# Performance work log

Hardware: AMD Instinct MI355X
Metric: run time of the kernel (lower is better)

Reference implementation:

```python
import jax, jax.numpy as jnp
import numpy as np

N, E, F_IN, F_HID, F_OUT, B = 50000, 800000, 128, 128, 128, 64
EPS = 1e-5


def _sage_conv(x, src, dst, w_l, b_l, w_r):
    # PyG SAGEConv (mean aggr): out = lin_l(mean_{j in N(i)} x_j) + lin_r(x_i)
    msg_sum = jax.ops.segment_sum(x[src], dst, num_segments=N)          # [N, F]
    deg = jax.ops.segment_sum(jnp.ones((src.shape[0],), x.dtype), dst, num_segments=N)
    agg = msg_sum / jnp.clip(deg, 1.0)[:, None]
    return agg @ w_l + b_l + x @ w_r


def _batch_norm(x, gamma, beta):
    # PyG BatchNorm (training): biased batch stats over the node dimension
    mu = jnp.mean(x, axis=0)
    var = jnp.mean((x - mu) ** 2, axis=0)
    return (x - mu) * jax.lax.rsqrt(var + EPS) * gamma + beta


def setup_inputs() -> dict:
    key = jax.random.key(0)
    ks = jax.random.split(key, 12)
    x = jax.random.normal(ks[0], (N, F_IN), jnp.float32)
    edge_index = jax.random.randint(ks[1], (2, E), 0, N, jnp.int64 if jax.config.jax_enable_x64 else jnp.int32)
    batch = jnp.sort(jax.random.randint(ks[2], (N,), 0, B))
    s1 = 1.0 / np.sqrt(F_IN)
    s2 = 1.0 / np.sqrt(F_HID)
    return {
        "x": x, "edge_index": edge_index, "batch": batch,
        "w_l1": jax.random.uniform(ks[3], (F_IN, F_HID), jnp.float32, -s1, s1),
        "b_l1": jax.random.uniform(ks[4], (F_HID,), jnp.float32, -s1, s1),
        "w_r1": jax.random.uniform(ks[5], (F_IN, F_HID), jnp.float32, -s1, s1),
        "g1": jnp.ones((F_HID,), jnp.float32),
        "beta1": jnp.zeros((F_HID,), jnp.float32),
        "w_l2": jax.random.uniform(ks[6], (F_HID, F_OUT), jnp.float32, -s2, s2),
        "b_l2": jax.random.uniform(ks[7], (F_OUT,), jnp.float32, -s2, s2),
        "w_r2": jax.random.uniform(ks[8], (F_HID, F_OUT), jnp.float32, -s2, s2),
        "g2": jnp.ones((F_OUT,), jnp.float32),
        "beta2": jnp.zeros((F_OUT,), jnp.float32),
    }


def reference(x, edge_index, batch, w_l1, b_l1, w_r1, g1, beta1, w_l2, b_l2, w_r2, g2, beta2):
    src, dst = edge_index[0], edge_index[1]
    h = jax.nn.relu(_batch_norm(_sage_conv(x, src, dst, w_l1, b_l1, w_r1), g1, beta1))
    h = jax.nn.relu(_batch_norm(_sage_conv(h, src, dst, w_l2, b_l2, w_r2), g2, beta2))
    # global_mean_pool over graph ids
    pooled = jax.ops.segment_sum(h, batch, num_segments=B)              # [B, F_OUT]
    cnt = jax.ops.segment_sum(jnp.ones((N,), h.dtype), batch, num_segments=B)
    return pooled / jnp.clip(cnt, 1.0)[:, None]
```

## Files before the change

### kernel.cpp

```cpp
#include <hip/hip_runtime.h>
#include <hip/hip_bf16.h>
#include <stdint.h>

typedef unsigned int uint32;
typedef unsigned short ushort16;

typedef __attribute__((ext_vector_type(8))) short short8;
typedef __attribute__((ext_vector_type(4))) float f32x4;

#define N_NODES 50000
#define N_EDGES 800000
#define FD      128
#define NGRAPH  64
#define MTILES  3125
#define NBK     196
#define GB      391
#define PCH     32
#define KCH     98

__device__ __forceinline__ float bf2f(ushort16 u){
  union { uint32 i; float f; } v; v.i = ((uint32)u) << 16; return v.f;
}
__device__ __forceinline__ float bf2f_lo(uint32 w){ union{uint32 i;float f;}v; v.i = w << 16; return v.f; }
__device__ __forceinline__ float bf2f_hi(uint32 w){ union{uint32 i;float f;}v; v.i = w & 0xffff0000u; return v.f; }
__device__ __forceinline__ ushort16 f2bf(float f){
  uint32 u = __float_as_uint(f);
  u += 0x7fffu + ((u >> 16) & 1u);
  return (ushort16)(u >> 16);
}

__device__ __forceinline__ int ld_idx(const void* p, uint32 is64, size_t i){
  return is64 ? (int)((const long long*)p)[i] : ((const int*)p)[i];
}
__device__ __forceinline__ float ld_f(const void* p, uint32 isf32, int i){
  return isf32 ? ((const float*)p)[i] : bf2f(((const ushort16*)p)[i]);
}


__global__ void detect_kernel(const uint32* __restrict__ xw, const uint32* __restrict__ eiw,
                              uint32* __restrict__ flags)
{
  int t = threadIdx.x;
  uint32 w = xw[t];
  uint32 e8 = (w >> 7) & 0xFFu;
  bool bf_like = (e8 >= 0x70u && e8 <= 0x82u);
  unsigned long long m = __ballot(bf_like);
  uint32 hi = (t < 8) ? eiw[2*t + 1] : 1u;
  unsigned long long z = __ballot(hi == 0u);
  if (t == 0){
    flags[0] = (__popcll(m) < 32) ? 1u : 0u;
    flags[1] = ((z & 0xFFull) == 0xFFull) ? 1u : 0u;
  }
}


__global__ __launch_bounds__(256) void pack_gseg_kernel(const void* __restrict__ ei,
    const void* __restrict__ batch, const uint32* __restrict__ flags,
    uint32* __restrict__ pack0, uint32* __restrict__ hist, uint32* __restrict__ gstart)
{
  uint32 is64 = flags[1];
  int tid = threadIdx.x;
  if (blockIdx.x < GB){
    __shared__ uint32 h[256];
    h[tid] = 0u;
    __syncthreads();
    int base = blockIdx.x*2048;
    for (int r = 0; r < 8; ++r){
      int i = base + r*256 + tid;
      if (i < N_EDGES){
        uint32 s = (uint32)ld_idx(ei, is64, i);
        uint32 d = (uint32)ld_idx(ei, is64, (size_t)N_EDGES + i);
        pack0[i] = (d << 16) | s;
        atomicAdd(&h[d >> 8], 1u);
      }
    }
    __syncthreads();
    hist[blockIdx.x*256 + tid] = h[tid];
  } else {
    int t = (blockIdx.x - GB)*256 + tid;
    if (t >= N_NODES) return;
    int b1 = ld_idx(batch, is64, t);
    int b0 = (t == 0) ? -1 : ld_idx(batch, is64, t - 1);
    for (int g = b0 + 1; g <= b1; ++g) gstart[g] = (uint32)t;
    if (t == N_NODES - 1)
      for (int g = b1 + 1; g <= NGRAPH; ++g) gstart[g] = (uint32)N_NODES;
  }
}

__global__ __launch_bounds__(1024) void scan_hist_kernel(const uint32* __restrict__ hist,
    uint32* __restrict__ off, uint32* __restrict__ bbase)
{
  __shared__ uint32 part[4][256];
  __shared__ uint32 lds[256];
  __shared__ uint32 bb[256];
  int tid = threadIdx.x;
  int seg = tid >> 8, b = tid & 255;
  int k0 = seg*KCH, k1 = (k0 + KCH < GB) ? k0 + KCH : GB;
  uint32 sum = 0;
  for (int k = k0; k < k1; ++k) sum += hist[k*256 + b];
  part[seg][b] = sum;
  __syncthreads();
  uint32 tot = 0, x = 0;
  if (seg == 0){
    tot = part[0][b] + part[1][b] + part[2][b] + part[3][b];
    x = tot; lds[b] = x;
  }
  __syncthreads();
  for (int o = 1; o < 256; o <<= 1){
    uint32 y = 0;
    if (seg == 0 && b >= o) y = lds[b - o];
    __syncthreads();
    if (seg == 0){ x += y; lds[b] = x; }
    __syncthreads();
  }
  if (seg == 0){
    uint32 base = x - tot;
    bb[b] = base;
    if (b <= NBK) bbase[b] = (b < NBK) ? base : (uint32)N_EDGES;
  }
  __syncthreads();
  uint32 run = bb[b];
  for (int s = 0; s < seg; ++s) run += part[s][b];
  for (int k = k0; k < k1; ++k){
    off[k*256 + b] = run;
    run += hist[k*256 + b];
  }
}

__global__ __launch_bounds__(256) void scatter_kernel(const uint32* __restrict__ pack0,
    const uint32* __restrict__ off, uint32* __restrict__ pack1)
{
  __shared__ uint32 cur[256];
  int tid = threadIdx.x;
  cur[tid] = off[blockIdx.x*256 + tid];
  __syncthreads();
  int base = blockIdx.x*2048;
  for (int r = 0; r < 8; ++r){
    int i = base + r*256 + tid;
    if (i < N_EDGES){
      uint32 p = pack0[i];
      uint32 pos = atomicAdd(&cur[p >> 24], 1u);
      pack1[pos] = p;
    }
  }
}

__global__ __launch_bounds__(256) void bucket_csr_kernel(const uint32* __restrict__ pack1,
    const uint32* __restrict__ bbase, uint32* __restrict__ rowstart,
    uint32* __restrict__ deg, ushort16* __restrict__ colidx)
{
  __shared__ uint32 cnt[256];
  __shared__ uint32 lds[256];
  __shared__ uint32 cur[256];
  int tid = threadIdx.x;
  int bk = blockIdx.x;
  uint32 e0 = bbase[bk], e1 = bbase[bk + 1];
  cnt[tid] = 0u;
  __syncthreads();
  for (uint32 i = e0 + tid; i < e1; i += 256)
    atomicAdd(&cnt[(pack1[i] >> 16) & 255u], 1u);
  __syncthreads();
  uint32 v = cnt[tid];
  uint32 x = v;
  lds[tid] = x; __syncthreads();
  for (int o = 1; o < 256; o <<= 1){
    uint32 y = (tid >= o) ? lds[tid - o] : 0u;
    __syncthreads();
    x += y; lds[tid] = x;
    __syncthreads();
  }
  uint32 start = e0 + x - v;
  int node = bk*256 + tid;
  if (node < N_NODES){ rowstart[node] = start; deg[node] = v; }
  cur[tid] = start;
  __syncthreads();
  for (uint32 i = e0 + tid; i < e1; i += 256){
    uint32 p = pack1[i];
    uint32 pos = atomicAdd(&cur[(p >> 16) & 255u], 1u);
    colidx[pos] = (ushort16)(p & 0xFFFFu);
  }
}


__global__ __launch_bounds__(256) void prep_kernel(const void* __restrict__ X,
    const void* __restrict__ WL1, const void* __restrict__ WR1,
    const void* __restrict__ WL2, const void* __restrict__ WR2,
    const uint32* __restrict__ flags, ushort16* __restrict__ xb, short* __restrict__ wfrag)
{
  uint32 isf32 = flags[0];
  if (blockIdx.x < 3125){
    if (!isf32) return;
    size_t e = ((size_t)blockIdx.x*256 + threadIdx.x)*8;
    const float* p = (const float*)X + e;
    float4 u = *(const float4*)p;
    float4 v = *(const float4*)(p + 4);
    uint4 o;
    o.x = (uint32)f2bf(u.x) | ((uint32)f2bf(u.y) << 16);
    o.y = (uint32)f2bf(u.z) | ((uint32)f2bf(u.w) << 16);
    o.z = (uint32)f2bf(v.x) | ((uint32)f2bf(v.y) << 16);
    o.w = (uint32)f2bf(v.z) | ((uint32)f2bf(v.w) << 16);
    *(uint4*)(xb + e) = o;
  } else {
    int t = (blockIdx.x - 3125)*256 + threadIdx.x;
    int layer = t >> 15;
    int r = t & 32767;
    int k = r >> 7, n = r & 127;
    const void* w = layer ? (k < 128 ? WL2 : WR2) : (k < 128 ? WL1 : WR1);
    int kk = k & 127;
    float wv = ld_f(w, isf32, kk*128 + n);
    int off = (((k >> 5)*8 + (n >> 4))*64 + (n & 15) + 16*((kk >> 3) & 3))*8 + (kk & 7);
    wfrag[layer*32768 + off] = (short)f2bf(wv);
  }
}


__device__ __forceinline__ void acc8(float* a, uint4 v, const float* s0, const float* h0, int APPLY){
  float f[8];
  f[0] = bf2f_lo(v.x); f[1] = bf2f_hi(v.x);
  f[2] = bf2f_lo(v.y); f[3] = bf2f_hi(v.y);
  f[4] = bf2f_lo(v.z); f[5] = bf2f_hi(v.z);
  f[6] = bf2f_lo(v.w); f[7] = bf2f_hi(v.w);
#pragma unroll
  for (int j = 0; j < 8; ++j)
    a[j] += APPLY ? fmaxf(f[j]*s0[j] + h0[j], 0.f) : f[j];
}

template<int APPLY>
__global__ __launch_bounds__(256) void agg_kernel(const ushort16* __restrict__ Xd,
    const void* __restrict__ Xraw,
    const uint32* __restrict__ rowstart, const uint32* __restrict__ deg,
    const ushort16* __restrict__ colidx,
    const float* __restrict__ sc, const float* __restrict__ sh,
    ushort16* __restrict__ out, const uint32* __restrict__ flags)
{
  const ushort16* X = (Xraw && !flags[0]) ? (const ushort16*)Xraw : Xd;
  int t = blockIdx.x*256 + threadIdx.x;
  int node = t >> 4;
  int l = t & 15;
  if (node >= N_NODES) return;
  uint32 st = rowstart[node];
  uint32 d  = deg[node];
  float s0[8], h0[8];
#pragma unroll
  for (int j = 0; j < 8; ++j){
    s0[j] = APPLY ? sc[l*8 + j] : 0.f;
    h0[j] = APPLY ? sh[l*8 + j] : 0.f;
  }
  float a[8];
#pragma unroll
  for (int j = 0; j < 8; ++j) a[j] = 0.f;
  uint32 i = 0;
  for (; i + 4 <= d; i += 4){
    uint32 c0 = colidx[st + i + 0];
    uint32 c1 = colidx[st + i + 1];
    uint32 c2 = colidx[st + i + 2];
    uint32 c3 = colidx[st + i + 3];
    uint4 v0 = *(const uint4*)(X + (size_t)c0*FD + l*8);
    uint4 v1 = *(const uint4*)(X + (size_t)c1*FD + l*8);
    uint4 v2 = *(const uint4*)(X + (size_t)c2*FD + l*8);
    uint4 v3 = *(const uint4*)(X + (size_t)c3*FD + l*8);
    acc8(a, v0, s0, h0, APPLY);
    acc8(a, v1, s0, h0, APPLY);
    acc8(a, v2, s0, h0, APPLY);
    acc8(a, v3, s0, h0, APPLY);
  }
  for (; i < d; ++i){
    uint32 c = colidx[st + i];
    uint4 v = *(const uint4*)(X + (size_t)c*FD + l*8);
    acc8(a, v, s0, h0, APPLY);
  }
  float inv = 1.f / fmaxf((float)d, 1.f);
  uint4 o;
  o.x = (uint32)f2bf(a[0]*inv) | ((uint32)f2bf(a[1]*inv) << 16);
  o.y = (uint32)f2bf(a[2]*inv) | ((uint32)f2bf(a[3]*inv) << 16);
  o.z = (uint32)f2bf(a[4]*inv) | ((uint32)f2bf(a[5]*inv) << 16);
  o.w = (uint32)f2bf(a[6]*inv) | ((uint32)f2bf(a[7]*inv) << 16);
  *(uint4*)(out + (size_t)node*FD + l*8) = o;
}


__device__ __forceinline__ short8 affine_relu8(short8 a, const float* sc, const float* sh, int koff){
  short8 r;
#pragma unroll
  for (int j = 0; j < 8; ++j){
    float v = bf2f((ushort16)a[j]) * sc[koff + j] + sh[koff + j];
    r[j] = (short)f2bf(fmaxf(v, 0.f));
  }
  return r;
}

template<int APPLY>
__global__ __launch_bounds__(256) void gemm_bn_kernel(
    const ushort16* __restrict__ A0, const ushort16* __restrict__ A1d,
    const void* __restrict__ A1raw,
    const short* __restrict__ wfrag, const void* __restrict__ bias,
    const uint32* __restrict__ flags,
    const float* __restrict__ sc, const float* __restrict__ sh,
    ushort16* __restrict__ hpre, float* __restrict__ bnpart)
{
  __shared__ float red[256];
  uint32 isf32 = flags[0];
  const ushort16* A1 = (A1raw && !isf32) ? (const ushort16*)A1raw : A1d;
  int tid = threadIdx.x;
  red[tid] = 0.f;
  int wave = tid >> 6, lane = tid & 63, lq = lane >> 4, lm = lane & 15;
  int mt0 = blockIdx.x*8 + wave*2;
  int mt1 = mt0 + 1;
  bool v0 = mt0 < MTILES, v1 = mt1 < MTILES;
  f32x4 acc0[8], acc1[8];
#pragma unroll
  for (int i = 0; i < 8; ++i){ acc0[i] = (f32x4){0.f,0.f,0.f,0.f}; acc1[i] = (f32x4){0.f,0.f,0.f,0.f}; }
  size_t m0 = (size_t)((v0 ? mt0 : 0)*16 + lm);
  size_t m1 = (size_t)((v1 ? mt1 : 0)*16 + lm);

#pragma unroll
  for (int ks = 0; ks < 8; ++ks){
    int koff = (ks & 3)*32 + lq*8;
    const short* srcp = (const short*)(ks < 4 ? A0 : A1);
    short8 a0 = *(const short8*)(srcp + m0*FD + koff);
    short8 a1 = *(const short8*)(srcp + m1*FD + koff);
    if (APPLY && ks >= 4){
      a0 = affine_relu8(a0, sc, sh, koff);
      a1 = affine_relu8(a1, sc, sh, koff);
    }
#pragma unroll
    for (int nt = 0; nt < 8; ++nt){
      short8 b = *(const short8*)&wfrag[((ks*8 + nt)*64 + lane)*8];
      acc0[nt] = __builtin_amdgcn_mfma_f32_16x16x32_bf16(a0, b, acc0[nt], 0, 0, 0);
      acc1[nt] = __builtin_amdgcn_mfma_f32_16x16x32_bf16(a1, b, acc1[nt], 0, 0, 0);
    }
  }

  __syncthreads();
#pragma unroll
  for (int nt = 0; nt < 8; ++nt){
    int colc = nt*16 + lm;
    float bb = ld_f(bias, isf32, colc);
    float s = 0.f, s2 = 0.f;
    if (v0){
      size_t nb = (size_t)(mt0*16 + lq*4);
#pragma unroll
      for (int r = 0; r < 4; ++r){
        float val = acc0[nt][r] + bb;
        hpre[(nb + r)*FD + colc] = f2bf(val);
        s += val; s2 += val*val;
      }
    }
    if (v1){
      size_t nb = (size_t)(mt1*16 + lq*4);
#pragma unroll
      for (int r = 0; r < 4; ++r){
        float val = acc1[nt][r] + bb;
        hpre[(nb + r)*FD + colc] = f2bf(val);
        s += val; s2 += val*val;
      }
    }
    s  += __shfl_xor(s, 16);  s  += __shfl_xor(s, 32);
    s2 += __shfl_xor(s2, 16); s2 += __shfl_xor(s2, 32);
    if (lq == 0){
      atomicAdd(&red[colc], s);
      atomicAdd(&red[128 + colc], s2);
    }
  }
  __syncthreads();
  bnpart[blockIdx.x*256 + tid] = red[tid];
}


__global__ __launch_bounds__(1024) void bn_final_kernel(const float* __restrict__ bnpart,
    const void* __restrict__ gamma, const void* __restrict__ beta,
    const uint32* __restrict__ flags, float* __restrict__ scale, float* __restrict__ shift)
{
  __shared__ float ls[1024], lq2[1024];
  uint32 isf32 = flags[0];
  int tid = threadIdx.x, f = tid & 127, seg = tid >> 7;
  float s = 0.f, q = 0.f;
  for (int b = seg; b < GB; b += 8){
    s += bnpart[b*256 + f];
    q += bnpart[b*256 + 128 + f];
  }
  ls[tid] = s; lq2[tid] = q;
  __syncthreads();
  if (tid < 128){
#pragma unroll
    for (int k = 1; k < 8; ++k){ s += ls[k*128 + f]; q += lq2[k*128 + f]; }
    const float invN = 1.0f / (float)N_NODES;
    float mu  = s * invN;
    float var = q * invN - mu*mu;
    float scv = ld_f(gamma, isf32, f) * rsqrtf(var + 1e-5f);
    scale[f] = scv;
    shift[f] = ld_f(beta, isf32, f) - mu * scv;
  }
}


__global__ __launch_bounds__(256) void pool_partial_kernel(const ushort16* __restrict__ hp,
    const float* __restrict__ scale, const float* __restrict__ shift,
    const uint32* __restrict__ gstart, float* __restrict__ pool_part)
{
  __shared__ float wred[4*16*8];
  int tid = threadIdx.x;
  int g = blockIdx.x >> 5, chunk = blockIdx.x & 31;
  int slot = tid >> 4, l = tid & 15;
  int wave = tid >> 6, lane = tid & 63;
  uint32 st = gstart[g], cnt = gstart[g+1] - st;
  uint32 per = (cnt + PCH - 1) >> 5;
  uint32 b0 = st + chunk*per;
  uint32 b1 = b0 + per;
  uint32 e1 = st + cnt;
  if (b1 > e1) b1 = e1;
  float s0[8], h0[8], a[8];
#pragma unroll
  for (int j = 0; j < 8; ++j){ s0[j] = scale[l*8 + j]; h0[j] = shift[l*8 + j]; a[j] = 0.f; }
  for (uint32 n = b0 + slot; n < b1; n += 16){
    const uint4 v = *(const uint4*)(hp + (size_t)n*FD + l*8);
    float f[8];
    f[0] = bf2f_lo(v.x); f[1] = bf2f_hi(v.x);
    f[2] = bf2f_lo(v.y); f[3] = bf2f_hi(v.y);
    f[4] = bf2f_lo(v.z); f[5] = bf2f_hi(v.z);
    f[6] = bf2f_lo(v.w); f[7] = bf2f_hi(v.w);
#pragma unroll
    for (int j = 0; j < 8; ++j) a[j] += fmaxf(f[j]*s0[j] + h0[j], 0.f);
  }
#pragma unroll
  for (int j = 0; j < 8; ++j){
    a[j] += __shfl_xor(a[j], 16);
    a[j] += __shfl_xor(a[j], 32);
  }
  if (lane < 16){
#pragma unroll
    for (int j = 0; j < 8; ++j) wred[(wave*16 + lane)*8 + j] = a[j];
  }
  __syncthreads();
  if (tid < 16){
    float r[8];
#pragma unroll
    for (int j = 0; j < 8; ++j)
      r[j] = wred[(0*16 + tid)*8 + j] + wred[(1*16 + tid)*8 + j]
           + wred[(2*16 + tid)*8 + j] + wred[(3*16 + tid)*8 + j];
    float* dst = pool_part + (size_t)blockIdx.x*FD + tid*8;
#pragma unroll
    for (int j = 0; j < 8; ++j) dst[j] = r[j];
  }
}

__global__ void pool_final_kernel(const float* __restrict__ pool_part,
    const uint32* __restrict__ gstart, void* __restrict__ out, const uint32* __restrict__ flags)
{
  uint32 isf32 = flags[0];
  int t = blockIdx.x*256 + threadIdx.x;
  int g = t >> 7, f = t & 127;
  float c = fmaxf((float)(gstart[g+1] - gstart[g]), 1.f);
  float v = 0.f;
#pragma unroll 8
  for (int ch = 0; ch < PCH; ++ch)
    v += pool_part[(size_t)(g*PCH + ch)*FD + f];
  v /= c;
  if (isf32) ((float*)out)[t] = v;
  else       ((ushort16*)out)[t] = f2bf(v);
}


extern "C" void kernel_launch(void* const* d_in, const int* in_sizes, int n_in,
                              void* d_out, int out_size, void* d_ws, size_t ws_size,
                              hipStream_t stream)
{
  const void* x   = d_in[0];
  const void* ei  = d_in[1];
  const void* bat = d_in[2];
  const void* wl1 = d_in[3];
  const void* bl1 = d_in[4];
  const void* wr1 = d_in[5];
  const void* g1  = d_in[6];
  const void* be1 = d_in[7];
  const void* wl2 = d_in[8];
  const void* bl2 = d_in[9];
  const void* wr2 = d_in[10];
  const void* g2  = d_in[11];
  const void* be2 = d_in[12];
  char* ws = (char*)d_ws;

  uint32* flags   = (uint32*)(ws + 0);
  uint32* gstart  = (uint32*)(ws + 64);
  uint32* bbase   = (uint32*)(ws + 384);
  float*  bnpart  = (float*) (ws + 1280);
  float*  scale1  = (float*) (ws + 401664);
  float*  shift1  = (float*) (ws + 402176);
  float*  scale2  = (float*) (ws + 402688);
  float*  shift2  = (float*) (ws + 403200);
  uint32* rowstart= (uint32*)(ws + 403712);
  uint32* deg     = (uint32*)(ws + 603712);
  ushort16* colidx= (ushort16*)(ws + 803712);
  short*  wfrag   = (short*) (ws + 2403712);
  ushort16* xb    = (ushort16*)(ws + 2534784);
  ushort16* aggb  = (ushort16*)(ws + 15334784);
  ushort16* hp1   = (ushort16*)(ws + 28134784);
  ushort16* hp2   = (ushort16*)(ws + 40934784);
  float*  ppart   = (float*) (ws + 53734784);
  uint32* pack0   = (uint32*)(ws + 28134784);
  uint32* pack1   = (uint32*)(ws + 31334784);
  uint32* hist    = (uint32*)(ws + 34534784);
  uint32* off     = (uint32*)(ws + 34935168);

  detect_kernel    <<<1,   64,  0, stream>>>((const uint32*)x, (const uint32*)ei, flags);

  pack_gseg_kernel <<<GB + 196, 256, 0, stream>>>(ei, bat, flags, pack0, hist, gstart);
  scan_hist_kernel <<<1,  1024, 0, stream>>>(hist, off, bbase);
  scatter_kernel   <<<GB,  256, 0, stream>>>(pack0, off, pack1);
  bucket_csr_kernel<<<NBK, 256, 0, stream>>>(pack1, bbase, rowstart, deg, colidx);

  prep_kernel      <<<3381, 256, 0, stream>>>(x, wl1, wr1, wl2, wr2, flags, xb, wfrag);

  agg_kernel<0>    <<<3125, 256, 0, stream>>>(xb, x, rowstart, deg, colidx, nullptr, nullptr, aggb, flags);
  gemm_bn_kernel<0><<<GB,   256, 0, stream>>>(aggb, xb, x, wfrag, bl1, flags, nullptr, nullptr, hp1, bnpart);
  bn_final_kernel  <<<1,   1024, 0, stream>>>(bnpart, g1, be1, flags, scale1, shift1);

  agg_kernel<1>    <<<3125, 256, 0, stream>>>(hp1, nullptr, rowstart, deg, colidx, scale1, shift1, aggb, flags);
  gemm_bn_kernel<1><<<GB,   256, 0, stream>>>(aggb, hp1, nullptr, wfrag + 32768, bl2, flags, scale1, shift1, hp2, bnpart);
  bn_final_kernel  <<<1,   1024, 0, stream>>>(bnpart, g2, be2, flags, scale2, shift2);

  pool_partial_kernel<<<NGRAPH*PCH, 256, 0, stream>>>(hp2, scale2, shift2, gstart, ppart);
  pool_final_kernel  <<<32,  256, 0, stream>>>(ppart, gstart, d_out, flags);
}
```

Baseline: 300.3 us.

## Fuse neighbor aggregation into MFMA GEMM and add separate BN-apply pass

Merges the gather-mean aggregation into the GEMM kernel: each wave gathers neighbor rows for its 16-node tile directly into MFMA A-fragments, so the aggregated matrix no longer goes through global memory. The layer-2 BatchNorm+ReLU is moved out of the aggregation into a standalone elementwise kernel that writes a normalized copy, which avoids re-applying the affine transform on every gathered neighbor. The BN finalize kernel is parallelized across 16 blocks with warp shuffles to handle twice as many partials. The trade-offs are one extra full pass over the hidden features, and per-lane gathers of four strided 16-byte chunks, which give less coalescing and less parallelism than the previous 16-lanes-per-node gather.

```diff
diff --git a/kernel.cpp b/kernel.cpp
--- a/kernel.cpp
+++ b/kernel.cpp
@@ -15,6 +15,7 @@
 #define MTILES  3125
 #define NBK     196
 #define GB      391
+#define GB2     782
 #define PCH     32
 #define KCH     98
 
@@ -214,120 +215,82 @@
 }
 
 
-__device__ __forceinline__ void acc8(float* a, uint4 v, const float* s0, const float* h0, int APPLY){
-  float f[8];
-  f[0] = bf2f_lo(v.x); f[1] = bf2f_hi(v.x);
-  f[2] = bf2f_lo(v.y); f[3] = bf2f_hi(v.y);
-  f[4] = bf2f_lo(v.z); f[5] = bf2f_hi(v.z);
-  f[6] = bf2f_lo(v.w); f[7] = bf2f_hi(v.w);
-#pragma unroll
-  for (int j = 0; j < 8; ++j)
-    a[j] += APPLY ? fmaxf(f[j]*s0[j] + h0[j], 0.f) : f[j];
-}
-
-template<int APPLY>
-__global__ __launch_bounds__(256) void agg_kernel(const ushort16* __restrict__ Xd,
-    const void* __restrict__ Xraw,
+__device__ __forceinline__ void acc8u(float* a, uint4 v){
+  a[0] += bf2f_lo(v.x); a[1] += bf2f_hi(v.x);
+  a[2] += bf2f_lo(v.y); a[3] += bf2f_hi(v.y);
+  a[4] += bf2f_lo(v.z); a[5] += bf2f_hi(v.z);
+  a[6] += bf2f_lo(v.w); a[7] += bf2f_hi(v.w);
+}
+
+__global__ __launch_bounds__(256) void fused_gemm_kernel(
+    const ushort16* __restrict__ Xd, const void* __restrict__ Xraw,
     const uint32* __restrict__ rowstart, const uint32* __restrict__ deg,
     const ushort16* __restrict__ colidx,
-    const float* __restrict__ sc, const float* __restrict__ sh,
-    ushort16* __restrict__ out, const uint32* __restrict__ flags)
-{
-  const ushort16* X = (Xraw && !flags[0]) ? (const ushort16*)Xraw : Xd;
-  int t = blockIdx.x*256 + threadIdx.x;
-  int node = t >> 4;
-  int l = t & 15;
-  if (node >= N_NODES) return;
-  uint32 st = rowstart[node];
-  uint32 d  = deg[node];
-  float s0[8], h0[8];
-#pragma unroll
-  for (int j = 0; j < 8; ++j){
-    s0[j] = APPLY ? sc[l*8 + j] : 0.f;
-    h0[j] = APPLY ? sh[l*8 + j] : 0.f;
-  }
-  float a[8];
-#pragma unroll
-  for (int j = 0; j < 8; ++j) a[j] = 0.f;
-  uint32 i = 0;
-  for (; i + 4 <= d; i += 4){
-    uint32 c0 = colidx[st + i + 0];
-    uint32 c1 = colidx[st + i + 1];
-    uint32 c2 = colidx[st + i + 2];
-    uint32 c3 = colidx[st + i + 3];
-    uint4 v0 = *(const uint4*)(X + (size_t)c0*FD + l*8);
-    uint4 v1 = *(const uint4*)(X + (size_t)c1*FD + l*8);
-    uint4 v2 = *(const uint4*)(X + (size_t)c2*FD + l*8);
-    uint4 v3 = *(const uint4*)(X + (size_t)c3*FD + l*8);
-    acc8(a, v0, s0, h0, APPLY);
-    acc8(a, v1, s0, h0, APPLY);
-    acc8(a, v2, s0, h0, APPLY);
-    acc8(a, v3, s0, h0, APPLY);
-  }
-  for (; i < d; ++i){
-    uint32 c = colidx[st + i];
-    uint4 v = *(const uint4*)(X + (size_t)c*FD + l*8);
-    acc8(a, v, s0, h0, APPLY);
-  }
-  float inv = 1.f / fmaxf((float)d, 1.f);
-  uint4 o;
-  o.x = (uint32)f2bf(a[0]*inv) | ((uint32)f2bf(a[1]*inv) << 16);
-  o.y = (uint32)f2bf(a[2]*inv) | ((uint32)f2bf(a[3]*inv) << 16);
-  o.z = (uint32)f2bf(a[4]*inv) | ((uint32)f2bf(a[5]*inv) << 16);
-  o.w = (uint32)f2bf(a[6]*inv) | ((uint32)f2bf(a[7]*inv) << 16);
-  *(uint4*)(out + (size_t)node*FD + l*8) = o;
-}
-
-
-__device__ __forceinline__ short8 affine_relu8(short8 a, const float* sc, const float* sh, int koff){
-  short8 r;
-#pragma unroll
-  for (int j = 0; j < 8; ++j){
-    float v = bf2f((ushort16)a[j]) * sc[koff + j] + sh[koff + j];
-    r[j] = (short)f2bf(fmaxf(v, 0.f));
-  }
-  return r;
-}
-
-template<int APPLY>
-__global__ __launch_bounds__(256) void gemm_bn_kernel(
-    const ushort16* __restrict__ A0, const ushort16* __restrict__ A1d,
-    const void* __restrict__ A1raw,
     const short* __restrict__ wfrag, const void* __restrict__ bias,
     const uint32* __restrict__ flags,
-    const float* __restrict__ sc, const float* __restrict__ sh,
     ushort16* __restrict__ hpre, float* __restrict__ bnpart)
 {
   __shared__ float red[256];
   uint32 isf32 = flags[0];
-  const ushort16* A1 = (A1raw && !isf32) ? (const ushort16*)A1raw : A1d;
+  const ushort16* X = (Xraw && !isf32) ? (const ushort16*)Xraw : Xd;
   int tid = threadIdx.x;
   red[tid] = 0.f;
   int wave = tid >> 6, lane = tid & 63, lq = lane >> 4, lm = lane & 15;
-  int mt0 = blockIdx.x*8 + wave*2;
-  int mt1 = mt0 + 1;
-  bool v0 = mt0 < MTILES, v1 = mt1 < MTILES;
-  f32x4 acc0[8], acc1[8];
-#pragma unroll
-  for (int i = 0; i < 8; ++i){ acc0[i] = (f32x4){0.f,0.f,0.f,0.f}; acc1[i] = (f32x4){0.f,0.f,0.f,0.f}; }
-  size_t m0 = (size_t)((v0 ? mt0 : 0)*16 + lm);
-  size_t m1 = (size_t)((v1 ? mt1 : 0)*16 + lm);
-
+  int mt = blockIdx.x*4 + wave;
+  bool valid = mt < MTILES;
+  int node = (valid ? mt : 0)*16 + lm;
+  uint32 st = rowstart[node];
+  uint32 d = valid ? deg[node] : 0u;
+
+  float ga[32];
+#pragma unroll
+  for (int i = 0; i < 32; ++i) ga[i] = 0.f;
+  const ushort16* Xl = X + lq*8;
+  uint32 j = 0;
+  for (; j + 2 <= d; j += 2){
+    uint32 c0 = colidx[st + j];
+    uint32 c1 = colidx[st + j + 1];
+    const ushort16* p0 = Xl + (size_t)c0*FD;
+    const ushort16* p1 = Xl + (size_t)c1*FD;
+    uint4 v00 = *(const uint4*)(p0);
+    uint4 v01 = *(const uint4*)(p0 + 32);
+    uint4 v02 = *(const uint4*)(p0 + 64);
+    uint4 v03 = *(const uint4*)(p0 + 96);
+    uint4 v10 = *(const uint4*)(p1);
+    uint4 v11 = *(const uint4*)(p1 + 32);
+    uint4 v12 = *(const uint4*)(p1 + 64);
+    uint4 v13 = *(const uint4*)(p1 + 96);
+    acc8u(&ga[0],  v00); acc8u(&ga[8],  v01); acc8u(&ga[16], v02); acc8u(&ga[24], v03);
+    acc8u(&ga[0],  v10); acc8u(&ga[8],  v11); acc8u(&ga[16], v12); acc8u(&ga[24], v13);
+  }
+  if (j < d){
+    uint32 c0 = colidx[st + j];
+    const ushort16* p0 = Xl + (size_t)c0*FD;
+    uint4 v00 = *(const uint4*)(p0);
+    uint4 v01 = *(const uint4*)(p0 + 32);
+    uint4 v02 = *(const uint4*)(p0 + 64);
+    uint4 v03 = *(const uint4*)(p0 + 96);
+    acc8u(&ga[0],  v00); acc8u(&ga[8],  v01); acc8u(&ga[16], v02); acc8u(&ga[24], v03);
+  }
+  float inv = 1.f / fmaxf((float)d, 1.f);
+  short8 af[4];
+#pragma unroll
+  for (int ks = 0; ks < 4; ++ks)
+#pragma unroll
+    for (int i = 0; i < 8; ++i)
+      af[ks][i] = (short)f2bf(ga[ks*8 + i]*inv);
+
+  f32x4 acc[8];
+#pragma unroll
+  for (int i = 0; i < 8; ++i) acc[i] = (f32x4){0.f,0.f,0.f,0.f};
+  const short* selfp = (const short*)(X + (size_t)node*FD) + lq*8;
 #pragma unroll
   for (int ks = 0; ks < 8; ++ks){
-    int koff = (ks & 3)*32 + lq*8;
-    const short* srcp = (const short*)(ks < 4 ? A0 : A1);
-    short8 a0 = *(const short8*)(srcp + m0*FD + koff);
-    short8 a1 = *(const short8*)(srcp + m1*FD + koff);
-    if (APPLY && ks >= 4){
-      a0 = affine_relu8(a0, sc, sh, koff);
-      a1 = affine_relu8(a1, sc, sh, koff);
-    }
+    short8 a = (ks < 4) ? af[ks] : *(const short8*)(selfp + (ks - 4)*32);
 #pragma unroll
     for (int nt = 0; nt < 8; ++nt){
       short8 b = *(const short8*)&wfrag[((ks*8 + nt)*64 + lane)*8];
-      acc0[nt] = __builtin_amdgcn_mfma_f32_16x16x32_bf16(a0, b, acc0[nt], 0, 0, 0);
-      acc1[nt] = __builtin_amdgcn_mfma_f32_16x16x32_bf16(a1, b, acc1[nt], 0, 0, 0);
+      acc[nt] = __builtin_amdgcn_mfma_f32_16x16x32_bf16(a, b, acc[nt], 0, 0, 0);
     }
   }
 
@@ -337,20 +300,11 @@
     int colc = nt*16 + lm;
     float bb = ld_f(bias, isf32, colc);
     float s = 0.f, s2 = 0.f;
-    if (v0){
-      size_t nb = (size_t)(mt0*16 + lq*4);
+    if (valid){
+      size_t nb = (size_t)mt*16 + lq*4;
 #pragma unroll
       for (int r = 0; r < 4; ++r){
-        float val = acc0[nt][r] + bb;
-        hpre[(nb + r)*FD + colc] = f2bf(val);
-        s += val; s2 += val*val;
-      }
-    }
-    if (v1){
-      size_t nb = (size_t)(mt1*16 + lq*4);
-#pragma unroll
-      for (int r = 0; r < 4; ++r){
-        float val = acc1[nt][r] + bb;
+        float val = acc[nt][r] + bb;
         hpre[(nb + r)*FD + colc] = f2bf(val);
         s += val; s2 += val*val;
       }
@@ -367,23 +321,25 @@
 }
 
 
-__global__ __launch_bounds__(1024) void bn_final_kernel(const float* __restrict__ bnpart,
+__global__ __launch_bounds__(256) void bn_final_kernel(const float* __restrict__ bnpart,
     const void* __restrict__ gamma, const void* __restrict__ beta,
     const uint32* __restrict__ flags, float* __restrict__ scale, float* __restrict__ shift)
 {
-  __shared__ float ls[1024], lq2[1024];
   uint32 isf32 = flags[0];
-  int tid = threadIdx.x, f = tid & 127, seg = tid >> 7;
+  int tid = threadIdx.x;
+  int f = blockIdx.x*8 + (tid >> 5);
+  int l = tid & 31;
   float s = 0.f, q = 0.f;
-  for (int b = seg; b < GB; b += 8){
+  for (int b = l; b < GB2; b += 32){
     s += bnpart[b*256 + f];
     q += bnpart[b*256 + 128 + f];
   }
-  ls[tid] = s; lq2[tid] = q;
-  __syncthreads();
-  if (tid < 128){
-#pragma unroll
-    for (int k = 1; k < 8; ++k){ s += ls[k*128 + f]; q += lq2[k*128 + f]; }
+#pragma unroll
+  for (int m = 16; m >= 1; m >>= 1){
+    s += __shfl_xor(s, m);
+    q += __shfl_xor(q, m);
+  }
+  if (l == 0){
     const float invN = 1.0f / (float)N_NODES;
     float mu  = s * invN;
     float var = q * invN - mu*mu;
@@ -391,6 +347,30 @@
     scale[f] = scv;
     shift[f] = ld_f(beta, isf32, f) - mu * scv;
   }
+}
+
+
+__global__ __launch_bounds__(256) void bn_apply_kernel(const ushort16* __restrict__ hp,
+    const float* __restrict__ scale, const float* __restrict__ shift, ushort16* __restrict__ z)
+{
+  size_t e = ((size_t)blockIdx.x*256 + threadIdx.x)*8;
+  int c = (int)(e & 127);
+  uint4 v = *(const uint4*)(hp + e);
+  float f[8];
+  f[0] = bf2f_lo(v.x); f[1] = bf2f_hi(v.x);
+  f[2] = bf2f_lo(v.y); f[3] = bf2f_hi(v.y);
+  f[4] = bf2f_lo(v.z); f[5] = bf2f_hi(v.z);
+  f[6] = bf2f_lo(v.w); f[7] = bf2f_hi(v.w);
+  ushort16 r[8];
+#pragma unroll
+  for (int j = 0; j < 8; ++j)
+    r[j] = f2bf(fmaxf(f[j]*scale[c + j] + shift[c + j], 0.f));
+  uint4 o;
+  o.x = (uint32)r[0] | ((uint32)r[1] << 16);
+  o.y = (uint32)r[2] | ((uint32)r[3] << 16);
+  o.z = (uint32)r[4] | ((uint32)r[5] << 16);
+  o.w = (uint32)r[6] | ((uint32)r[7] << 16);
+  *(uint4*)(z + e) = o;
 }
 
 
@@ -484,23 +464,23 @@
   uint32* gstart  = (uint32*)(ws + 64);
   uint32* bbase   = (uint32*)(ws + 384);
   float*  bnpart  = (float*) (ws + 1280);
-  float*  scale1  = (float*) (ws + 401664);
-  float*  shift1  = (float*) (ws + 402176);
-  float*  scale2  = (float*) (ws + 402688);
-  float*  shift2  = (float*) (ws + 403200);
-  uint32* rowstart= (uint32*)(ws + 403712);
-  uint32* deg     = (uint32*)(ws + 603712);
-  ushort16* colidx= (ushort16*)(ws + 803712);
-  short*  wfrag   = (short*) (ws + 2403712);
-  ushort16* xb    = (ushort16*)(ws + 2534784);
-  ushort16* aggb  = (ushort16*)(ws + 15334784);
-  ushort16* hp1   = (ushort16*)(ws + 28134784);
-  ushort16* hp2   = (ushort16*)(ws + 40934784);
-  float*  ppart   = (float*) (ws + 53734784);
-  uint32* pack0   = (uint32*)(ws + 28134784);
-  uint32* pack1   = (uint32*)(ws + 31334784);
-  uint32* hist    = (uint32*)(ws + 34534784);
-  uint32* off     = (uint32*)(ws + 34935168);
+  float*  scale1  = (float*) (ws + 802048);
+  float*  shift1  = (float*) (ws + 802560);
+  float*  scale2  = (float*) (ws + 803072);
+  float*  shift2  = (float*) (ws + 803584);
+  uint32* rowstart= (uint32*)(ws + 804096);
+  uint32* deg     = (uint32*)(ws + 1004096);
+  ushort16* colidx= (ushort16*)(ws + 1204096);
+  short*  wfrag   = (short*) (ws + 2804096);
+  ushort16* xb    = (ushort16*)(ws + 2935168);
+  ushort16* z1    = (ushort16*)(ws + 15735168);
+  ushort16* hp1   = (ushort16*)(ws + 28535168);
+  ushort16* hp2   = (ushort16*)(ws + 41335168);
+  uint32* pack0   = (uint32*)(ws + 28535168);
+  uint32* pack1   = (uint32*)(ws + 31735168);
+  uint32* hist    = (uint32*)(ws + 34935168);
+  uint32* off     = (uint32*)(ws + 35335552);
+  float*  ppart   = (float*) (ws + 28535168);
 
   detect_kernel    <<<1,   64,  0, stream>>>((const uint32*)x, (const uint32*)ei, flags);
 
@@ -511,13 +491,14 @@
 
   prep_kernel      <<<3381, 256, 0, stream>>>(x, wl1, wr1, wl2, wr2, flags, xb, wfrag);
 
-  agg_kernel<0>    <<<3125, 256, 0, stream>>>(xb, x, rowstart, deg, colidx, nullptr, nullptr, aggb, flags);
-  gemm_bn_kernel<0><<<GB,   256, 0, stream>>>(aggb, xb, x, wfrag, bl1, flags, nullptr, nullptr, hp1, bnpart);
-  bn_final_kernel  <<<1,   1024, 0, stream>>>(bnpart, g1, be1, flags, scale1, shift1);
-
-  agg_kernel<1>    <<<3125, 256, 0, stream>>>(hp1, nullptr, rowstart, deg, colidx, scale1, shift1, aggb, flags);
-  gemm_bn_kernel<1><<<GB,   256, 0, stream>>>(aggb, hp1, nullptr, wfrag + 32768, bl2, flags, scale1, shift1, hp2, bnpart);
-  bn_final_kernel  <<<1,   1024, 0, stream>>>(bnpart, g2, be2, flags, scale2, shift2);
+  fused_gemm_kernel<<<GB2, 256, 0, stream>>>(xb, x, rowstart, deg, colidx,
+                                             wfrag, bl1, flags, hp1, bnpart);
+  bn_final_kernel  <<<16,  256, 0, stream>>>(bnpart, g1, be1, flags, scale1, shift1);
+  bn_apply_kernel  <<<3125,256, 0, stream>>>(hp1, scale1, shift1, z1);
+
+  fused_gemm_kernel<<<GB2, 256, 0, stream>>>(z1, nullptr, rowstart, deg, colidx,
+                                             wfrag + 32768, bl2, flags, hp2, bnpart);
+  bn_final_kernel  <<<16,  256, 0, stream>>>(bnpart, g2, be2, flags, scale2, shift2);
 
   pool_partial_kernel<<<NGRAPH*PCH, 256, 0, stream>>>(hp2, scale2, shift2, gstart, ppart);
   pool_final_kernel  <<<32,  256, 0, stream>>>(ppart, gstart, d_out, flags);
```

Result: slower. 331.9 us (+10.5%).
